# Performance work log

Measured on AMD Instinct MI355X. Metric: run time of the kernel, lower is better.

## Reference

```python
import jax, jax.numpy as jnp
import numpy as np

B, C, L, H, W = 8, 512, 256, 64, 64  # batch, in_channels, latent_channels, spatial
EPS = 1e-5


def setup_inputs() -> dict:
    key = jax.random.key(0)
    ks = jax.random.split(key, 16)

    def n(k, shape, s=1.0):
        return jax.random.normal(k, shape, dtype=jnp.float32) * s

    return {
        "x_f": n(ks[0], (B, C, H, W)),
        "x_g": n(ks[1], (B, C, H, W)),
        "x_h": n(ks[2], (B, C, H, W)),
        "x_t": n(ks[3], (B, C, H, W)),
        # stacked per-stream params, stream order (f, g, h, t)
        "Wk": n(ks[4], (4, L, C), 0.02), "bk": n(ks[5], (4, L), 0.02),
        "gk": jnp.ones((4, L), jnp.float32), "betak": jnp.zeros((4, L), jnp.float32),
        "mk": n(ks[6], (4, L), 0.1),
        "vk": jax.random.uniform(ks[7], (4, L), jnp.float32, 0.5, 1.5),
        "Wq": n(ks[8], (4, L, C), 0.02), "bq": n(ks[9], (4, L), 0.02),
        "gq": jnp.ones((4, L), jnp.float32), "betaq": jnp.zeros((4, L), jnp.float32),
        "mq": n(ks[10], (4, L), 0.1),
        "vq": jax.random.uniform(ks[11], (4, L), jnp.float32, 0.5, 1.5),
        "Wd": n(ks[12], (4, L, C), 0.02), "bd": n(ks[13], (4, L), 0.02),
        "Wu": n(ks[14], (4, C, L), 0.02), "bu": n(ks[15], (4, C), 0.02),
    }


def _conv1x1(x, Wt, b):
    # x: [4,B,C,H,W], Wt: [4,L,C] -> [4,B,L,H,W]
    return jnp.einsum('sbchw,slc->sblhw', x, Wt) + b[:, None, :, None, None]


def _bn_relu(y, g, beta, m, v):
    scale = (g / jnp.sqrt(v + EPS))[:, None, :, None, None]
    return jax.nn.relu((y - m[:, None, :, None, None]) * scale + beta[:, None, :, None, None])


def reference(x_f, x_g, x_h, x_t, Wk, bk, gk, betak, mk, vk,
              Wq, bq, gq, betaq, mq, vq, Wd, bd, Wu, bu):
    x = jnp.stack([x_f, x_g, x_h, x_t])  # [4,B,C,H,W]
    b_, c_, h_, w_ = x_f.shape
    l_ = Wk.shape[1]

    k = _bn_relu(_conv1x1(x, Wk, bk), gk, betak, mk, vk)   # [4,B,L,H,W]
    q = _bn_relu(_conv1x1(x, Wq, bq), gq, betaq, mq, vq)   # [4,B,L,H,W]
    val = _conv1x1(x, Wd, bd)                              # [4,B,L,H,W]

    # faithful torch .view on contiguous NCHW: raw reshape, not transpose
    kv = k.reshape(4, b_, h_, w_, l_)
    qv = q.reshape(4, b_, h_, w_, l_)
    vv = val.reshape(4, b_, h_, w_, l_)

    q4 = jnp.moveaxis(qv, 0, 3)  # [B,H,W,4,L]  (cat dim4 then permute)
    k4 = jnp.moveaxis(kv, 0, 4)  # [B,H,W,L,4]  (cat dim4)
    v4 = jnp.moveaxis(vv, 0, 3)  # [B,H,W,4,L]

    sim = jnp.einsum('bhwsl,bhwlt->bhwst', q4, k4) * (l_ ** -0.5)  # [B,H,W,4,4]
    attn = jax.nn.softmax(sim, axis=-1)
    ctx = jnp.einsum('bhwst,bhwtl->bhwsl', attn, v4)               # [B,H,W,4,L]

    ctx = jnp.moveaxis(ctx, 3, 0)  # [4,B,H,W,L]
    up = jnp.einsum('sbhwl,scl->sbchw', ctx, Wu) + bu[:, None, :, None, None]
    out = x + up  # [4,B,C,H,W]
    return (out[0], out[1], out[2], out[3])
```

## Files before the change

### kernel.cpp

```cpp
#include <hip/hip_runtime.h>

#define B_   8
#define C_   512
#define L_   256
#define HW_  4096
#define EPSV 1e-5f

typedef short  short8   __attribute__((ext_vector_type(8)));
typedef float  floatx4  __attribute__((ext_vector_type(4)));
typedef unsigned short ushort8v __attribute__((ext_vector_type(8)));

__device__ __forceinline__ unsigned short f2bf(float f) {
    unsigned u = __float_as_uint(f);
    u = (u + 0x7FFF + ((u >> 16) & 1)) >> 16;
    return (unsigned short)u;
}
__device__ __forceinline__ float bf2f(unsigned short h) {
    return __uint_as_float(((unsigned)h) << 16);
}

#define AS3 __attribute__((address_space(3)))
#define AS1 __attribute__((address_space(1)))
__device__ __forceinline__ void async_cp16(const void* g, void* l) {
    __builtin_amdgcn_global_load_lds((const AS1 void*)g, (AS3 void*)l, 16, 0, 0);
}

template<int STRIDE>
__device__ __forceinline__ void stage_tile(
    const unsigned short* __restrict__ Abase,
    const unsigned short* __restrict__ Bbase,
    unsigned short* smem, int bufBase, int tid, int m0, int n0, int k0)
{
#pragma unroll
    for (int it = 0; it < 2; ++it) {
        int slot = tid + it * 256;
        int row  = slot >> 2;
        int pos  = slot & 3;
        int kg   = pos ^ ((row >> 1) & 3);
        async_cp16(Abase + (size_t)(m0 + row) * STRIDE + k0 + kg * 8,
                   &smem[bufBase + slot * 8]);
        async_cp16(Bbase + (size_t)(n0 + row) * STRIDE + k0 + kg * 8,
                   &smem[bufBase + 4096 + slot * 8]);
    }
}

__global__ __launch_bounds__(256) void prep_kernel(
    const float* __restrict__ Wk, const float* __restrict__ bk,
    const float* __restrict__ gk, const float* __restrict__ betak,
    const float* __restrict__ mk, const float* __restrict__ vk,
    const float* __restrict__ Wq, const float* __restrict__ bq,
    const float* __restrict__ gq, const float* __restrict__ betaq,
    const float* __restrict__ mq, const float* __restrict__ vq,
    const float* __restrict__ Wd, const float* __restrict__ bd,
    const float* __restrict__ Wu,
    unsigned short* __restrict__ Aall, float* __restrict__ biasA,
    unsigned short* __restrict__ Wub)
{
    const int NA = 4 * 768 * C_;
    const int NW = 4 * C_ * L_;
    const int NB = 4 * 768;
    int idx = blockIdx.x * 256 + threadIdx.x;
    if (idx < NA) {
        int s = idx / (768 * C_);
        int rem = idx % (768 * C_);
        int r = rem / C_, c = rem % C_;
        float w;
        if (r < 256) {
            int sl = s * L_ + r;
            float sc = gk[sl] * rsqrtf(vk[sl] + EPSV);
            w = Wk[(size_t)sl * C_ + c] * sc;
        } else if (r < 512) {
            int sl = s * L_ + (r - 256);
            float sc = gq[sl] * rsqrtf(vq[sl] + EPSV);
            w = Wq[(size_t)sl * C_ + c] * sc;
        } else {
            int sl = s * L_ + (r - 512);
            w = Wd[(size_t)sl * C_ + c];
        }
        Aall[idx] = f2bf(w);
    } else if (idx < NA + NW) {
        int i = idx - NA;
        Wub[i] = f2bf(Wu[i]);
    } else if (idx < NA + NW + NB) {
        int i = idx - NA - NW;
        int s = i / 768, r = i % 768;
        float bv;
        if (r < 256) {
            int sl = s * L_ + r;
            float sc = gk[sl] * rsqrtf(vk[sl] + EPSV);
            bv = (bk[sl] - mk[sl]) * sc + betak[sl];
        } else if (r < 512) {
            int sl = s * L_ + (r - 256);
            float sc = gq[sl] * rsqrtf(vq[sl] + EPSV);
            bv = (bq[sl] - mq[sl]) * sc + betaq[sl];
        } else {
            bv = bd[s * L_ + (r - 512)];
        }
        biasA[i] = bv;
    }
}

__global__ __launch_bounds__(256) void transpose_kernel(
    const float* __restrict__ xf, const float* __restrict__ xg,
    const float* __restrict__ xh, const float* __restrict__ xt,
    unsigned short* __restrict__ xT)
{
    __shared__ unsigned short tile[64][66];
    int p0 = blockIdx.x * 64;
    int c0 = blockIdx.y * 64;
    int sb = blockIdx.z;
    int s = sb >> 3, b = sb & 7;
    const float* x = (s == 0) ? xf : (s == 1) ? xg : (s == 2) ? xh : xt;
    const float* xb = x + (size_t)b * C_ * HW_;
    int tid = threadIdx.x;
    int g = tid >> 4;
    int t = tid & 15;
    int p4 = t * 4;
#pragma unroll
    for (int i = 0; i < 4; ++i) {
        int r = g + i * 16;
        float4 v = *(const float4*)&xb[(size_t)(c0 + r) * HW_ + p0 + p4];
        tile[r][p4 + 0] = f2bf(v.x);
        tile[r][p4 + 1] = f2bf(v.y);
        tile[r][p4 + 2] = f2bf(v.z);
        tile[r][p4 + 3] = f2bf(v.w);
    }
    __syncthreads();
    unsigned short* o = xT + (size_t)sb * HW_ * C_;
    int c4 = t * 4;
#pragma unroll
    for (int i = 0; i < 4; ++i) {
        int p = g + i * 16;
        ushort4 u;
        u.x = tile[c4 + 0][p];
        u.y = tile[c4 + 1][p];
        u.z = tile[c4 + 2][p];
        u.w = tile[c4 + 3][p];
        *(ushort4*)&o[(size_t)(p0 + p) * C_ + c0 + c4] = u;
    }
}

__global__ __launch_bounds__(256) void down_gemm(
    const unsigned short* __restrict__ Aall, const float* __restrict__ biasA,
    const unsigned short* __restrict__ xT,
    unsigned short* __restrict__ KQV)
{
    __shared__ unsigned short smem[16384] __attribute__((aligned(16)));
    int n0 = blockIdx.x * 128;
    int m0 = blockIdx.y * 128;
    int sb = blockIdx.z;
    int s = sb >> 3;
    int tid = threadIdx.x;
    int lane = tid & 63, wave = tid >> 6;
    int wm = (wave & 1) * 64, wn = (wave >> 1) * 64;
    int quad = lane >> 4, l16 = lane & 15;
    const unsigned short* Abase = Aall + (size_t)s * 768 * C_;
    const unsigned short* Bbase = xT + (size_t)sb * HW_ * C_;

    floatx4 acc[4][4];
#pragma unroll
    for (int i = 0; i < 4; ++i)
#pragma unroll
        for (int j = 0; j < 4; ++j) acc[i][j] = (floatx4){0.f, 0.f, 0.f, 0.f};

    stage_tile<C_>(Abase, Bbase, smem, 0, tid, m0, n0, 0);
    __syncthreads();

    int cur = 0;
#pragma unroll 2
    for (int kt = 0; kt < C_ / 32; ++kt) {
        int nxt = cur ^ 8192;
        if (kt + 1 < C_ / 32)
            stage_tile<C_>(Abase, Bbase, smem, nxt, tid, m0, n0, (kt + 1) * 32);
        const unsigned short* At = &smem[cur];
        const unsigned short* Bt = &smem[cur + 4096];
        short8 a[4], bb[4];
#pragma unroll
        for (int mi = 0; mi < 4; ++mi) {
            int rr = wm + mi * 16 + l16;
            int pos = quad ^ ((rr >> 1) & 3);
            a[mi] = *(const short8*)&At[rr * 32 + pos * 8];
        }
#pragma unroll
        for (int ni = 0; ni < 4; ++ni) {
            int rr = wn + ni * 16 + l16;
            int pos = quad ^ ((rr >> 1) & 3);
            bb[ni] = *(const short8*)&Bt[rr * 32 + pos * 8];
        }
#pragma unroll
        for (int mi = 0; mi < 4; ++mi)
#pragma unroll
            for (int ni = 0; ni < 4; ++ni)
                acc[mi][ni] = __builtin_amdgcn_mfma_f32_16x16x32_bf16(
                    a[mi], bb[ni], acc[mi][ni], 0, 0, 0);
        __syncthreads();
        cur = nxt;
    }

    unsigned short* Ot = smem;
#pragma unroll
    for (int mi = 0; mi < 4; ++mi) {
        int rbase = wm + mi * 16 + quad * 4;
#pragma unroll
        for (int r = 0; r < 4; ++r) {
            int row = rbase + r;
            int gm = m0 + row;
            float bias = biasA[s * 768 + gm];
            bool doRelu = (gm < 512);
#pragma unroll
            for (int ni = 0; ni < 4; ++ni) {
                int col = wn + ni * 16 + l16;
                float v = acc[mi][ni][r] + bias;
                if (doRelu) v = fmaxf(v, 0.f);
                Ot[row * 128 + col] = f2bf(v);
            }
        }
    }
    __syncthreads();
#pragma unroll
    for (int i = 0; i < 8; ++i) {
        int fo = (tid + i * 256) * 8;
        int row = fo >> 7;
        int col = fo & 127;
        *(ushort8v*)&KQV[((size_t)sb * 768 + m0 + row) * HW_ + n0 + col] =
            *(const ushort8v*)&Ot[fo];
    }
}

__global__ __launch_bounds__(256) void attn_kernel(
    const unsigned short* __restrict__ KQV, unsigned short* __restrict__ Ctx)
{
    int gw = (blockIdx.x * 256 + threadIdx.x) >> 6;
    int lane = threadIdx.x & 63;
    int b = gw >> 12;
    int j = gw & 4095;

    float qf[4][4], kf[4][4], vf[4][4];
#pragma unroll
    for (int s = 0; s < 4; ++s) {
        size_t sbase = (size_t)(s * 8 + b) * (768 * HW_) + (size_t)j * 256 + lane * 4;
        ushort4 ku = *(const ushort4*)(KQV + sbase);
        ushort4 qu = *(const ushort4*)(KQV + sbase + (size_t)256 * HW_);
        ushort4 vu = *(const ushort4*)(KQV + sbase + (size_t)512 * HW_);
        qf[s][0] = bf2f(qu.x); qf[s][1] = bf2f(qu.y); qf[s][2] = bf2f(qu.z); qf[s][3] = bf2f(qu.w);
        kf[s][0] = bf2f(ku.x); kf[s][1] = bf2f(ku.y); kf[s][2] = bf2f(ku.z); kf[s][3] = bf2f(ku.w);
        vf[s][0] = bf2f(vu.x); vf[s][1] = bf2f(vu.y); vf[s][2] = bf2f(vu.z); vf[s][3] = bf2f(vu.w);
    }
    float p[4][4];
#pragma unroll
    for (int s = 0; s < 4; ++s)
#pragma unroll
        for (int t = 0; t < 4; ++t) {
            float acc = 0.f;
#pragma unroll
            for (int e = 0; e < 4; ++e) acc += qf[s][e] * kf[t][e];
            p[s][t] = acc;
        }
#pragma unroll
    for (int off = 1; off < 64; off <<= 1)
#pragma unroll
        for (int s = 0; s < 4; ++s)
#pragma unroll
            for (int t = 0; t < 4; ++t)
                p[s][t] += __shfl_xor(p[s][t], off, 64);

    float at[4][4];
#pragma unroll
    for (int s = 0; s < 4; ++s) {
        float m = -1e30f;
#pragma unroll
        for (int t = 0; t < 4; ++t) { p[s][t] *= 0.0625f; m = fmaxf(m, p[s][t]); }
        float sm = 0.f;
#pragma unroll
        for (int t = 0; t < 4; ++t) { at[s][t] = __expf(p[s][t] - m); sm += at[s][t]; }
        float inv = 1.f / sm;
#pragma unroll
        for (int t = 0; t < 4; ++t) at[s][t] *= inv;
    }
#pragma unroll
    for (int s = 0; s < 4; ++s) {
        float c[4] = {0.f, 0.f, 0.f, 0.f};
#pragma unroll
        for (int t = 0; t < 4; ++t)
#pragma unroll
            for (int e = 0; e < 4; ++e) c[e] += at[s][t] * vf[t][e];
        ushort4 o;
        o.x = f2bf(c[0]); o.y = f2bf(c[1]); o.z = f2bf(c[2]); o.w = f2bf(c[3]);
        *(ushort4*)(Ctx + (size_t)(s * 8 + b) * (L_ * HW_) + (size_t)j * 256 + lane * 4) = o;
    }
}

__global__ __launch_bounds__(256) void up_gemm(
    const unsigned short* __restrict__ Wub, const float* __restrict__ bu,
    const unsigned short* __restrict__ Ctx,
    const float* __restrict__ xf, const float* __restrict__ xg,
    const float* __restrict__ xh, const float* __restrict__ xt,
    float* __restrict__ out)
{
    __shared__ unsigned short smem[16384] __attribute__((aligned(16)));
    int n0 = blockIdx.x * 128;
    int m0 = blockIdx.y * 128;
    int sb = blockIdx.z;
    int s = sb >> 3, b = sb & 7;
    int tid = threadIdx.x;
    int lane = tid & 63, wave = tid >> 6;
    int wm = (wave & 1) * 64, wn = (wave >> 1) * 64;
    int quad = lane >> 4, l16 = lane & 15;
    const unsigned short* Abase = Wub + (size_t)s * C_ * L_;
    const unsigned short* Bbase = Ctx + (size_t)sb * HW_ * L_;

    floatx4 acc[4][4];
#pragma unroll
    for (int i = 0; i < 4; ++i)
#pragma unroll
        for (int j = 0; j < 4; ++j) acc[i][j] = (floatx4){0.f, 0.f, 0.f, 0.f};

    stage_tile<L_>(Abase, Bbase, smem, 0, tid, m0, n0, 0);
    __syncthreads();

    int cur = 0;
#pragma unroll 2
    for (int kt = 0; kt < L_ / 32; ++kt) {
        int nxt = cur ^ 8192;
        if (kt + 1 < L_ / 32)
            stage_tile<L_>(Abase, Bbase, smem, nxt, tid, m0, n0, (kt + 1) * 32);
        const unsigned short* At = &smem[cur];
        const unsigned short* Bt = &smem[cur + 4096];
        short8 a[4], bb[4];
#pragma unroll
        for (int mi = 0; mi < 4; ++mi) {
            int rr = wm + mi * 16 + l16;
            int pos = quad ^ ((rr >> 1) & 3);
            a[mi] = *(const short8*)&At[rr * 32 + pos * 8];
        }
#pragma unroll
        for (int ni = 0; ni < 4; ++ni) {
            int rr = wn + ni * 16 + l16;
            int pos = quad ^ ((rr >> 1) & 3);
            bb[ni] = *(const short8*)&Bt[rr * 32 + pos * 8];
        }
#pragma unroll
        for (int mi = 0; mi < 4; ++mi)
#pragma unroll
            for (int ni = 0; ni < 4; ++ni)
                acc[mi][ni] = __builtin_amdgcn_mfma_f32_16x16x32_bf16(
                    a[mi], bb[ni], acc[mi][ni], 0, 0, 0);
        __syncthreads();
        cur = nxt;
    }

    const float* x = (s == 0) ? xf : (s == 1) ? xg : (s == 2) ? xh : xt;
    const float* xb = x + (size_t)b * C_ * HW_;
#pragma unroll
    for (int mi = 0; mi < 4; ++mi) {
        int gmBase = m0 + wm + mi * 16 + quad * 4;
#pragma unroll
        for (int r = 0; r < 4; ++r) {
            int gm = gmBase + r;
            float bias = bu[s * C_ + gm];
#pragma unroll
            for (int ni = 0; ni < 4; ++ni) {
                int gn = n0 + wn + ni * 16 + l16;
                float rx = __builtin_nontemporal_load(&xb[(size_t)gm * HW_ + gn]);
                float v = acc[mi][ni][r] + bias + rx;
                __builtin_nontemporal_store(v, &out[((size_t)sb * C_ + gm) * HW_ + gn]);
            }
        }
    }
}

extern "C" void kernel_launch(void* const* d_in, const int* in_sizes, int n_in,
                              void* d_out, int out_size, void* d_ws, size_t ws_size,
                              hipStream_t stream) {
    (void)in_sizes; (void)n_in; (void)out_size; (void)ws_size;
    const float* xf    = (const float*)d_in[0];
    const float* xg    = (const float*)d_in[1];
    const float* xh    = (const float*)d_in[2];
    const float* xt    = (const float*)d_in[3];
    const float* Wk    = (const float*)d_in[4];
    const float* bk    = (const float*)d_in[5];
    const float* gk    = (const float*)d_in[6];
    const float* betak = (const float*)d_in[7];
    const float* mk    = (const float*)d_in[8];
    const float* vk    = (const float*)d_in[9];
    const float* Wq    = (const float*)d_in[10];
    const float* bq    = (const float*)d_in[11];
    const float* gq    = (const float*)d_in[12];
    const float* betaq = (const float*)d_in[13];
    const float* mq    = (const float*)d_in[14];
    const float* vq    = (const float*)d_in[15];
    const float* Wd    = (const float*)d_in[16];
    const float* bd    = (const float*)d_in[17];
    const float* Wu    = (const float*)d_in[18];
    const float* bu    = (const float*)d_in[19];

    char* ws = (char*)d_ws;
    unsigned short* Aall  = (unsigned short*)(ws + 0);
    float*          biasA = (float*)(ws + 3145728);
    unsigned short* Wub   = (unsigned short*)(ws + 3158016);
    unsigned short* xT    = (unsigned short*)(ws + 4206592);
    unsigned short* KQV   = (unsigned short*)(ws + 138424320);
    unsigned short* Ctx   = (unsigned short*)(ws + 339750912);

    prep_kernel<<<dim3(8204), 256, 0, stream>>>(
        Wk, bk, gk, betak, mk, vk, Wq, bq, gq, betaq, mq, vq, Wd, bd, Wu,
        Aall, biasA, Wub);
    transpose_kernel<<<dim3(64, 8, 32), 256, 0, stream>>>(xf, xg, xh, xt, xT);
    down_gemm<<<dim3(32, 6, 32), 256, 0, stream>>>(Aall, biasA, xT, KQV);
    attn_kernel<<<dim3(8192), 256, 0, stream>>>(KQV, Ctx);
    up_gemm<<<dim3(32, 4, 32), 256, 0, stream>>>(Wub, bu, Ctx, xf, xg, xh, xt,
                                                 (float*)d_out);
}
```

Measured before the change: 806.6 us.

## Triple-buffer LDS staging in down and up GEMMs with one barrier per step

Both GEMM kernels move from a double-buffered async global-to-LDS pipeline to a three-stage ring. Two tiles are prefetched ahead, and each step waits only on the older loads with vmcnt(4) plus a single raw s_barrier, instead of a full __syncthreads after compute. The aim is to hide global load latency better and cut barrier stalls. LDS per block grows from 32KB to 48KB, which may lower occupancy. Correctness depends on the hand-set vmcnt count matching the four async copies issued per tile.

```diff
diff --git a/kernel.cpp b/kernel.cpp
--- a/kernel.cpp
+++ b/kernel.cpp
@@ -42,6 +42,31 @@
         async_cp16(Bbase + (size_t)(n0 + row) * STRIDE + k0 + kg * 8,
                    &smem[bufBase + 4096 + slot * 8]);
     }
+}
+
+__device__ __forceinline__ void mma_step(
+    const unsigned short* __restrict__ At, const unsigned short* __restrict__ Bt,
+    floatx4 (&acc)[4][4], int wm, int wn, int quad, int l16)
+{
+    short8 a[4], bb[4];
+#pragma unroll
+    for (int mi = 0; mi < 4; ++mi) {
+        int rr = wm + mi * 16 + l16;
+        int pos = quad ^ ((rr >> 1) & 3);
+        a[mi] = *(const short8*)&At[rr * 32 + pos * 8];
+    }
+#pragma unroll
+    for (int ni = 0; ni < 4; ++ni) {
+        int rr = wn + ni * 16 + l16;
+        int pos = quad ^ ((rr >> 1) & 3);
+        bb[ni] = *(const short8*)&Bt[rr * 32 + pos * 8];
+    }
+#pragma unroll
+    for (int mi = 0; mi < 4; ++mi)
+#pragma unroll
+        for (int ni = 0; ni < 4; ++ni)
+            acc[mi][ni] = __builtin_amdgcn_mfma_f32_16x16x32_bf16(
+                a[mi], bb[ni], acc[mi][ni], 0, 0, 0);
 }
 
 __global__ __launch_bounds__(256) void prep_kernel(
@@ -145,7 +170,7 @@
     const unsigned short* __restrict__ xT,
     unsigned short* __restrict__ KQV)
 {
-    __shared__ unsigned short smem[16384] __attribute__((aligned(16)));
+    __shared__ unsigned short smem[24576] __attribute__((aligned(16)));
     int n0 = blockIdx.x * 128;
     int m0 = blockIdx.y * 128;
     int sb = blockIdx.z;
@@ -163,39 +188,28 @@
 #pragma unroll
         for (int j = 0; j < 4; ++j) acc[i][j] = (floatx4){0.f, 0.f, 0.f, 0.f};
 
-    stage_tile<C_>(Abase, Bbase, smem, 0, tid, m0, n0, 0);
+    const int NT = C_ / 32;
+    stage_tile<C_>(Abase, Bbase, smem, 0,    tid, m0, n0, 0);
+    stage_tile<C_>(Abase, Bbase, smem, 8192, tid, m0, n0, 32);
+
+    for (int k = 0; k < NT - 1; ++k) {
+        asm volatile("s_waitcnt vmcnt(4)" ::: "memory");
+        __builtin_amdgcn_s_barrier();
+        __builtin_amdgcn_sched_barrier(0);
+        if (k + 2 < NT)
+            stage_tile<C_>(Abase, Bbase, smem, ((k + 2) % 3) * 8192,
+                           tid, m0, n0, (k + 2) * 32);
+        const unsigned short* At = &smem[(k % 3) * 8192];
+        mma_step(At, At + 4096, acc, wm, wn, quad, l16);
+    }
+    asm volatile("s_waitcnt vmcnt(0)" ::: "memory");
+    __builtin_amdgcn_s_barrier();
+    __builtin_amdgcn_sched_barrier(0);
+    {
+        const unsigned short* At = &smem[((NT - 1) % 3) * 8192];
+        mma_step(At, At + 4096, acc, wm, wn, quad, l16);
+    }
     __syncthreads();
-
-    int cur = 0;
-#pragma unroll 2
-    for (int kt = 0; kt < C_ / 32; ++kt) {
-        int nxt = cur ^ 8192;
-        if (kt + 1 < C_ / 32)
-            stage_tile<C_>(Abase, Bbase, smem, nxt, tid, m0, n0, (kt + 1) * 32);
-        const unsigned short* At = &smem[cur];
-        const unsigned short* Bt = &smem[cur + 4096];
-        short8 a[4], bb[4];
-#pragma unroll
-        for (int mi = 0; mi < 4; ++mi) {
-            int rr = wm + mi * 16 + l16;
-            int pos = quad ^ ((rr >> 1) & 3);
-            a[mi] = *(const short8*)&At[rr * 32 + pos * 8];
-        }
-#pragma unroll
-        for (int ni = 0; ni < 4; ++ni) {
-            int rr = wn + ni * 16 + l16;
-            int pos = quad ^ ((rr >> 1) & 3);
-            bb[ni] = *(const short8*)&Bt[rr * 32 + pos * 8];
-        }
-#pragma unroll
-        for (int mi = 0; mi < 4; ++mi)
-#pragma unroll
-            for (int ni = 0; ni < 4; ++ni)
-                acc[mi][ni] = __builtin_amdgcn_mfma_f32_16x16x32_bf16(
-                    a[mi], bb[ni], acc[mi][ni], 0, 0, 0);
-        __syncthreads();
-        cur = nxt;
-    }
 
     unsigned short* Ot = smem;
 #pragma unroll
@@ -297,7 +311,7 @@
     const float* __restrict__ xh, const float* __restrict__ xt,
     float* __restrict__ out)
 {
-    __shared__ unsigned short smem[16384] __attribute__((aligned(16)));
+    __shared__ unsigned short smem[24576] __attribute__((aligned(16)));
     int n0 = blockIdx.x * 128;
     int m0 = blockIdx.y * 128;
     int sb = blockIdx.z;
@@ -315,38 +329,26 @@
 #pragma unroll
         for (int j = 0; j < 4; ++j) acc[i][j] = (floatx4){0.f, 0.f, 0.f, 0.f};
 
-    stage_tile<L_>(Abase, Bbase, smem, 0, tid, m0, n0, 0);
-    __syncthreads();
-
-    int cur = 0;
-#pragma unroll 2
-    for (int kt = 0; kt < L_ / 32; ++kt) {
-        int nxt = cur ^ 8192;
-        if (kt + 1 < L_ / 32)
-            stage_tile<L_>(Abase, Bbase, smem, nxt, tid, m0, n0, (kt + 1) * 32);
-        const unsigned short* At = &smem[cur];
-        const unsigned short* Bt = &smem[cur + 4096];
-        short8 a[4], bb[4];
-#pragma unroll
-        for (int mi = 0; mi < 4; ++mi) {
-            int rr = wm + mi * 16 + l16;
-            int pos = quad ^ ((rr >> 1) & 3);
-            a[mi] = *(const short8*)&At[rr * 32 + pos * 8];
-        }
-#pragma unroll
-        for (int ni = 0; ni < 4; ++ni) {
-            int rr = wn + ni * 16 + l16;
-            int pos = quad ^ ((rr >> 1) & 3);
-            bb[ni] = *(const short8*)&Bt[rr * 32 + pos * 8];
-        }
-#pragma unroll
-        for (int mi = 0; mi < 4; ++mi)
-#pragma unroll
-            for (int ni = 0; ni < 4; ++ni)
-                acc[mi][ni] = __builtin_amdgcn_mfma_f32_16x16x32_bf16(
-                    a[mi], bb[ni], acc[mi][ni], 0, 0, 0);
-        __syncthreads();
-        cur = nxt;
+    const int NT = L_ / 32;
+    stage_tile<L_>(Abase, Bbase, smem, 0,    tid, m0, n0, 0);
+    stage_tile<L_>(Abase, Bbase, smem, 8192, tid, m0, n0, 32);
+
+    for (int k = 0; k < NT - 1; ++k) {
+        asm volatile("s_waitcnt vmcnt(4)" ::: "memory");
+        __builtin_amdgcn_s_barrier();
+        __builtin_amdgcn_sched_barrier(0);
+        if (k + 2 < NT)
+            stage_tile<L_>(Abase, Bbase, smem, ((k + 2) % 3) * 8192,
+                           tid, m0, n0, (k + 2) * 32);
+        const unsigned short* At = &smem[(k % 3) * 8192];
+        mma_step(At, At + 4096, acc, wm, wn, quad, l16);
+    }
+    asm volatile("s_waitcnt vmcnt(0)" ::: "memory");
+    __builtin_amdgcn_s_barrier();
+    __builtin_amdgcn_sched_barrier(0);
+    {
+        const unsigned short* At = &smem[((NT - 1) % 3) * 8192];
+        mma_step(At, At + 4096, acc, wm, wn, quad, l16);
     }
 
     const float* x = (s == 0) ? xf : (s == 1) ? xg : (s == 2) ? xh : xt;
```

New measurement: 814.9 us. No clear change (+1.0%).
